# Performance work log

Measured on AMD Instinct MI355X. Metric: run time of the kernel, lower is better.

Reference implementation:

```python
import jax, jax.numpy as jnp
import numpy as np

N_CLASSES = 5
IGNORE = 255
IMAX = 32  # max instance index value (indexes in [1, IMAX])


def setup_inputs() -> dict:
    key = jax.random.key(0)
    k1, k2, k3 = jax.random.split(key, 3)
    B, D, H, W = 8, 128, 512, 512
    feature_out = jax.random.normal(k1, (B, D, H, W), dtype=jnp.float32)
    labels = jax.random.randint(k2, (B, H, W), 0, N_CLASSES).astype(jnp.int32)
    indexes = jax.random.randint(k3, (B, H, W), 1, IMAX + 1).astype(jnp.int32)
    return {"feature_out": feature_out, "labels": labels, "indexes": indexes}


def _lintra(feature_out, labels, indexes):
    # Semantics of the torch module (sort + boundary detection + python loops),
    # re-expressed as a fused segment reduction:
    #  - per-image segments are (label, instance-index) pairs among non-ignore pixels
    #  - segments with key==0 (ignore) or with a single pixel are excluded
    #  - per (image, class): instance means F [K, D], ret = mean_{i,j,d} |F_i - F_j|
    #    (includes i==j diagonal, as in the original KxK broadcast), then smooth-L1
    #  - final loss = mean over all (image, class) losses / B
    B, D, H, W = feature_out.shape
    feats = jnp.transpose(feature_out, (0, 2, 3, 1)).reshape(B * H * W, D)
    lab = labels.reshape(B, -1)
    idx = indexes.reshape(B, -1)
    valid = lab != IGNORE
    lab = jnp.where(valid, lab, 0)
    idx = jnp.where(valid, idx, 0)
    S = N_CLASSES * (IMAX + 1)
    seg = lab * (IMAX + 1) + idx                      # 0 marks ignore pixels
    gseg = (seg + jnp.arange(B, dtype=seg.dtype)[:, None] * S).reshape(-1)
    sums = jax.ops.segment_sum(feats, gseg, num_segments=B * S)
    counts = jax.ops.segment_sum(jnp.ones((B * H * W,), feats.dtype), gseg,
                                 num_segments=B * S)
    means = sums / jnp.maximum(counts, 1.0)[:, None]
    means = means.reshape(B, N_CLASSES, IMAX + 1, D)
    counts = counts.reshape(B, N_CLASSES, IMAX + 1)
    inc = counts >= 2.0                               # singleton segments skipped
    inc = inc.at[:, :, 0].set(False)                  # key==0 slot (ignore) skipped
    incf = inc.astype(means.dtype)                    # [B, C, I]
    # intra-class pairwise |F_i - F_j|, masked to included instances
    diff = jnp.abs(means[:, :, :, None, :] - means[:, :, None, :, :])  # [B,C,I,I,D]
    pair = incf[:, :, :, None] * incf[:, :, None, :]                   # [B,C,I,I]
    ssum = jnp.einsum('bcijd,bcij->bc', diff, pair)
    K = incf.sum(-1)                                   # instances per (image,class)
    ret = jnp.where(K > 0, ssum / jnp.maximum(K * K * D, 1.0), 0.0)
    loss_bc = jnp.where(ret < 1.0, 0.5 * ret * ret, ret - 0.5)
    has = (K > 0).astype(ret.dtype)
    n = has.sum()
    total = jnp.where(n > 0, (loss_bc * has).sum() / jnp.maximum(n, 1.0), 0.0)
    return (total / B).reshape(1)


def reference(feature_out, labels, indexes):
    return _lintra(feature_out, labels, indexes)
```

## Files before the change

kernel.cpp:

```cpp
#include <hip/hip_runtime.h>
#include <stdint.h>

#define NC 5
#define IMAXP1 33
#define SEGS 165
#define SEGS_PAD 192
#define MT 6
#define HW_ (512 * 512)
#define IGNORE_L 255
#define KCHUNK 2048
#define NSUP (KCHUNK / 64)

typedef __attribute__((ext_vector_type(8))) short short8v;
typedef __attribute__((ext_vector_type(16))) float f32x16;
typedef __attribute__((ext_vector_type(2))) unsigned short u16x2;
typedef __attribute__((ext_vector_type(2))) float float2v;
typedef __attribute__((ext_vector_type(2))) __bf16 bf16x2;
typedef __attribute__((ext_vector_type(2))) unsigned long long u64x2;

__global__ __launch_bounds__(256) void seg_count_kernel(
    const int* __restrict__ labels, const int* __restrict__ indexes,
    uint8_t* __restrict__ seg, unsigned* __restrict__ counts,
    int pix_per_block) {
  __shared__ unsigned hist[SEGS];
  for (int i = threadIdx.x; i < SEGS; i += blockDim.x) hist[i] = 0u;
  __syncthreads();

  const long long base = (long long)blockIdx.x * pix_per_block;
  const int b = (int)(base / HW_);
  const int nvec = pix_per_block / 4;
  const int4* lab4 = (const int4*)(labels + base);
  const int4* idx4 = (const int4*)(indexes + base);
  uchar4* seg4 = (uchar4*)(seg + base);

  for (int k = threadIdx.x; k < nvec; k += blockDim.x) {
    int4 l = lab4[k];
    int4 ix = idx4[k];
    int s0 = (l.x == IGNORE_L) ? 0 : l.x * IMAXP1 + ix.x;
    int s1 = (l.y == IGNORE_L) ? 0 : l.y * IMAXP1 + ix.y;
    int s2 = (l.z == IGNORE_L) ? 0 : l.z * IMAXP1 + ix.z;
    int s3 = (l.w == IGNORE_L) ? 0 : l.w * IMAXP1 + ix.w;
    uchar4 sv;
    sv.x = (unsigned char)s0; sv.y = (unsigned char)s1;
    sv.z = (unsigned char)s2; sv.w = (unsigned char)s3;
    seg4[k] = sv;
    atomicAdd(&hist[s0], 1u);
    atomicAdd(&hist[s1], 1u);
    atomicAdd(&hist[s2], 1u);
    atomicAdd(&hist[s3], 1u);
  }
  __syncthreads();
  for (int i = threadIdx.x; i < SEGS; i += blockDim.x)
    if (hist[i]) atomicAdd(&counts[b * SEGS + i], hist[i]);
}

struct SS {
  float4 f[8];
  u64x2 g0, g1;
};

__global__ __launch_bounds__(256, 2) void segsum_mfma_kernel(
    const float* __restrict__ feat, const uint8_t* __restrict__ seg,
    float* __restrict__ sums, int chunks_per_img) {
  __shared__ unsigned long long sseg8[KCHUNK / 8];
  const int b = blockIdx.x / chunks_per_img;
  const int chunk = blockIdx.x % chunks_per_img;
  const int pbase = chunk * KCHUNK;

  const unsigned long long* gseg8 =
      (const unsigned long long*)(seg + (size_t)b * HW_ + pbase);
  sseg8[threadIdx.x] = gseg8[threadIdx.x];
  __syncthreads();

  const int l = threadIdx.x & 63;
  const int w = threadIdx.x >> 6;
  const int lane31 = l & 31;
  const int hi = l >> 5;
  const int ch = w * 32 + lane31;

  const float4* fp4 =
      (const float4*)(feat + ((size_t)b * 128 + ch) * HW_ + pbase) + hi * 8;
  const uint8_t* sp = (const uint8_t*)sseg8 + hi * 32;

  const unsigned lane2 = (unsigned)lane31 | ((unsigned)lane31 << 16);

  f32x16 acc[MT];
  #pragma unroll
  for (int m = 0; m < MT; ++m) acc[m] = (f32x16)(0.f);

  #define LOAD_SS(dst, s)                                             \
    do {                                                              \
      _Pragma("unroll") for (int i = 0; i < 8; ++i)                   \
          (dst).f[i] = fp4[(size_t)(s)*16 + i];                       \
      const u64x2* sp2 = (const u64x2*)(sp + (s)*64);                 \
      (dst).g0 = sp2[0];                                              \
      (dst).g1 = sp2[1];                                              \
    } while (0)

  #define KSTEP(f0, f1, sb)                                           \
    do {                                                              \
      unsigned svp[4];                                                \
      _Pragma("unroll") for (int j = 0; j < 4; ++j) {                 \
        unsigned lo8 = (unsigned)(((sb) >> (16 * j)) & 0xFFull);      \
        unsigned hi8 = (unsigned)(((sb) >> (16 * j + 8)) & 0xFFull);  \
        svp[j] = (lo8 | (hi8 << 16)) ^ lane2;                         \
      }                                                               \
      float fs[8] = {(f0).x, (f0).y, (f0).z, (f0).w,                  \
                     (f1).x, (f1).y, (f1).z, (f1).w};                 \
      union { unsigned u[4]; short8v v; } bhi, blo;                   \
      _Pragma("unroll") for (int j = 0; j < 4; ++j) {                 \
        float2v f2 = {fs[2 * j], fs[2 * j + 1]};                      \
        bf16x2 h2 = __builtin_convertvector(f2, bf16x2);              \
        unsigned hb = __builtin_bit_cast(unsigned, h2);               \
        bhi.u[j] = hb;                                                \
        float fh0 = __builtin_bit_cast(float, hb << 16);              \
        float fh1 = __builtin_bit_cast(float, hb & 0xFFFF0000u);      \
        float2v l2 = {f2.x - fh0, f2.y - fh1};                        \
        bf16x2 lo2 = __builtin_convertvector(l2, bf16x2);             \
        blo.u[j] = __builtin_bit_cast(unsigned, lo2);                 \
      }                                                               \
      _Pragma("unroll") for (int m = 0; m < MT; ++m) {                \
        unsigned m2 = (unsigned)(m * 32) | ((unsigned)(m * 32) << 16);\
        union { unsigned u[4]; short8v v; } a;                        \
        _Pragma("unroll") for (int j = 0; j < 4; ++j) {               \
          u16x2 y = __builtin_bit_cast(u16x2, svp[j] ^ m2);           \
          u16x2 nz = __builtin_elementwise_min(y, (u16x2)(unsigned short)1); \
          u16x2 msk = nz - (u16x2)(unsigned short)1;                  \
          u16x2 av = msk & (u16x2)(unsigned short)0x3F80;             \
          a.u[j] = __builtin_bit_cast(unsigned, av);                  \
        }                                                             \
        acc[m] = __builtin_amdgcn_mfma_f32_32x32x16_bf16(a.v, bhi.v,  \
                                                         acc[m], 0, 0, 0); \
        acc[m] = __builtin_amdgcn_mfma_f32_32x32x16_bf16(a.v, blo.v,  \
                                                         acc[m], 0, 0, 0); \
      }                                                               \
    } while (0)

  #define COMPUTE_SS(src)                                             \
    do {                                                              \
      KSTEP((src).f[0], (src).f[1], (src).g0.x);                      \
      KSTEP((src).f[2], (src).f[3], (src).g0.y);                      \
      KSTEP((src).f[4], (src).f[5], (src).g1.x);                      \
      KSTEP((src).f[6], (src).f[7], (src).g1.y);                      \
    } while (0)

  SS bufA, bufB;
  LOAD_SS(bufA, 0);
  for (int s = 0; s < NSUP; s += 2) {
    LOAD_SS(bufB, s + 1);
    COMPUTE_SS(bufA);
    if (s + 2 < NSUP) LOAD_SS(bufA, s + 2);
    COMPUTE_SS(bufB);
  }

  #pragma unroll
  for (int m = 0; m < MT; ++m) {
    #pragma unroll
    for (int r = 0; r < 16; ++r) {
      int s = m * 32 + (r & 3) + 8 * (r >> 2) + 4 * hi;
      float v = acc[m][r];
      if (v != 0.f)
        atomicAdd(&sums[((size_t)b * SEGS_PAD + s) * 128 + ch], v);
    }
  }
}

__global__ __launch_bounds__(256) void pairloss_kernel(
    const float* __restrict__ sums, const unsigned* __restrict__ counts,
    float* __restrict__ loss_sum, unsigned* __restrict__ nvalid, int D) {
  const int b = blockIdx.x / NC;
  const int c = blockIdx.x % NC;

  __shared__ float sh_mean[32 * 128];
  __shared__ float sh_cnt[IMAXP1];
  __shared__ int list[IMAXP1];
  __shared__ int Ksh;
  __shared__ uchar2 pairs[32 * 31 / 2];
  __shared__ double wred[4];

  if (threadIdx.x == 0) {
    int K = 0;
    for (int i = 1; i < IMAXP1; ++i) {
      unsigned cnt = counts[b * SEGS + c * IMAXP1 + i];
      if (cnt >= 2u) {
        list[K] = i;
        sh_cnt[K] = (float)cnt;
        ++K;
      }
    }
    Ksh = K;
    int p = 0;
    for (int i = 0; i < K; ++i)
      for (int j = i + 1; j < K; ++j) {
        pairs[p].x = (unsigned char)i;
        pairs[p].y = (unsigned char)j;
        ++p;
      }
  }
  __syncthreads();
  const int K = Ksh;
  if (K == 0) return;

  for (int idx = threadIdx.x; idx < K * D; idx += blockDim.x) {
    int k = idx / 128, d = idx % 128;
    int s = c * IMAXP1 + list[k];
    sh_mean[k * 128 + d] =
        sums[((size_t)b * SEGS_PAD + s) * D + d] / sh_cnt[k];
  }
  __syncthreads();

  const int npairs = K * (K - 1) / 2;
  const int total = npairs * 128;
  float local = 0.f;
  for (int idx = threadIdx.x; idx < total; idx += blockDim.x) {
    int p = idx >> 7, d = idx & 127;
    int i = pairs[p].x, j = pairs[p].y;
    local += fabsf(sh_mean[i * 128 + d] - sh_mean[j * 128 + d]);
  }

  double v = (double)local;
  #pragma unroll
  for (int off = 32; off; off >>= 1) v += __shfl_down(v, off, 64);
  const int wave = threadIdx.x >> 6;
  if ((threadIdx.x & 63) == 0) wred[wave] = v;
  __syncthreads();
  if (threadIdx.x == 0) {
    double ssum = 2.0 * (wred[0] + wred[1] + wred[2] + wred[3]);
    double ret = ssum / ((double)K * (double)K * (double)D);
    double loss = (ret < 1.0) ? 0.5 * ret * ret : ret - 0.5;
    atomicAdd(loss_sum, (float)loss);
    atomicAdd(nvalid, 1u);
  }
}

__global__ void finalize_kernel(const float* __restrict__ loss_sum,
                                const unsigned* __restrict__ nvalid,
                                float* __restrict__ out, int B) {
  if (threadIdx.x == 0) {
    unsigned n = *nvalid;
    out[0] = n ? (*loss_sum / (float)n) / (float)B : 0.f;
  }
}

extern "C" void kernel_launch(void* const* d_in, const int* in_sizes, int n_in,
                              void* d_out, int out_size, void* d_ws,
                              size_t ws_size, hipStream_t stream) {
  const float* feat = (const float*)d_in[0];
  const int* labels = (const int*)d_in[1];
  const int* indexes = (const int*)d_in[2];

  const int npix_total = in_sizes[1];
  const int B = npix_total / HW_;
  const int D = in_sizes[0] / npix_total;

  uint8_t* seg = (uint8_t*)d_ws;
  size_t off = ((size_t)npix_total + 255) & ~(size_t)255;
  float* sums = (float*)((char*)d_ws + off);
  size_t sums_bytes = (size_t)B * SEGS_PAD * D * sizeof(float);
  unsigned* counts = (unsigned*)((char*)d_ws + off + sums_bytes);
  size_t counts_bytes = (size_t)B * SEGS * sizeof(unsigned);
  float* loss_sum = (float*)((char*)d_ws + off + sums_bytes + counts_bytes);
  unsigned* nvalid = (unsigned*)(loss_sum + 1);

  hipMemsetAsync(sums, 0, sums_bytes + counts_bytes + 2 * sizeof(unsigned),
                 stream);

  const int pix_per_block = 4096;
  seg_count_kernel<<<npix_total / pix_per_block, 256, 0, stream>>>(
      labels, indexes, seg, counts, pix_per_block);

  const int cpi = HW_ / KCHUNK;
  segsum_mfma_kernel<<<B * cpi, 256, 0, stream>>>(feat, seg, sums, cpi);

  pairloss_kernel<<<B * NC, 256, 0, stream>>>(sums, counts, loss_sum, nvalid,
                                              D);
  finalize_kernel<<<1, 64, 0, stream>>>(loss_sum, nvalid, (float*)d_out, B);
}
```

Before: 334.9 us.

## Replace global atomic segment accumulation with per-block partials and a reduction kernel

The MFMA segment-sum kernel now writes each block's full 192x128 accumulator tile to a per-block partials buffer instead of issuing global float atomics, and a new kernel sums the partials per image. The chunk size doubles so there are half as many blocks and partial tiles. This removes atomic contention on the shared sums array and the memset of sums, at the cost of writing and re-reading about 50 MB of partials plus an extra launch.

```diff
diff --git a/kernel.cpp b/kernel.cpp
--- a/kernel.cpp
+++ b/kernel.cpp
@@ -8,8 +8,9 @@
 #define MT 6
 #define HW_ (512 * 512)
 #define IGNORE_L 255
-#define KCHUNK 2048
+#define KCHUNK 4096
 #define NSUP (KCHUNK / 64)
+#define TILE (SEGS_PAD * 128)
 
 typedef __attribute__((ext_vector_type(8))) short short8v;
 typedef __attribute__((ext_vector_type(16))) float f32x16;
@@ -61,7 +62,7 @@
 
 __global__ __launch_bounds__(256, 2) void segsum_mfma_kernel(
     const float* __restrict__ feat, const uint8_t* __restrict__ seg,
-    float* __restrict__ sums, int chunks_per_img) {
+    float* __restrict__ partials, int chunks_per_img) {
   __shared__ unsigned long long sseg8[KCHUNK / 8];
   const int b = blockIdx.x / chunks_per_img;
   const int chunk = blockIdx.x % chunks_per_img;
@@ -69,7 +70,7 @@
 
   const unsigned long long* gseg8 =
       (const unsigned long long*)(seg + (size_t)b * HW_ + pbase);
-  sseg8[threadIdx.x] = gseg8[threadIdx.x];
+  for (int i = threadIdx.x; i < KCHUNK / 8; i += 256) sseg8[i] = gseg8[i];
   __syncthreads();
 
   const int l = threadIdx.x & 63;
@@ -153,16 +154,26 @@
     COMPUTE_SS(bufB);
   }
 
+  float* pb = partials + (size_t)blockIdx.x * TILE;
   #pragma unroll
   for (int m = 0; m < MT; ++m) {
     #pragma unroll
     for (int r = 0; r < 16; ++r) {
       int s = m * 32 + (r & 3) + 8 * (r >> 2) + 4 * hi;
-      float v = acc[m][r];
-      if (v != 0.f)
-        atomicAdd(&sums[((size_t)b * SEGS_PAD + s) * 128 + ch], v);
+      pb[s * 128 + ch] = acc[m][r];
     }
   }
+}
+
+__global__ __launch_bounds__(256) void reduce_partials_kernel(
+    const float* __restrict__ partials, float* __restrict__ sums,
+    int chunks_per_img) {
+  const int o = blockIdx.x * 256 + threadIdx.x;
+  const int b = blockIdx.y;
+  const float* p = partials + (size_t)b * chunks_per_img * TILE + o;
+  float t = 0.f;
+  for (int c = 0; c < chunks_per_img; ++c) t += p[(size_t)c * TILE];
+  sums[(size_t)b * TILE + o] = t;
 }
 
 __global__ __launch_bounds__(256) void pairloss_kernel(
@@ -205,7 +216,7 @@
     int k = idx / 128, d = idx % 128;
     int s = c * IMAXP1 + list[k];
     sh_mean[k * 128 + d] =
-        sums[((size_t)b * SEGS_PAD + s) * D + d] / sh_cnt[k];
+        sums[(size_t)b * TILE + s * 128 + d] / sh_cnt[k];
   }
   __syncthreads();
 
@@ -252,25 +263,31 @@
   const int npix_total = in_sizes[1];
   const int B = npix_total / HW_;
   const int D = in_sizes[0] / npix_total;
+  const int cpi = HW_ / KCHUNK;
+  const int nblocks = B * cpi;
 
   uint8_t* seg = (uint8_t*)d_ws;
   size_t off = ((size_t)npix_total + 255) & ~(size_t)255;
-  float* sums = (float*)((char*)d_ws + off);
-  size_t sums_bytes = (size_t)B * SEGS_PAD * D * sizeof(float);
-  unsigned* counts = (unsigned*)((char*)d_ws + off + sums_bytes);
+  float* partials = (float*)((char*)d_ws + off);
+  size_t part_bytes = (size_t)nblocks * TILE * sizeof(float);
+  float* sums = (float*)((char*)d_ws + off + part_bytes);
+  size_t sums_bytes = (size_t)B * TILE * sizeof(float);
+  unsigned* counts = (unsigned*)((char*)d_ws + off + part_bytes + sums_bytes);
   size_t counts_bytes = (size_t)B * SEGS * sizeof(unsigned);
-  float* loss_sum = (float*)((char*)d_ws + off + sums_bytes + counts_bytes);
+  float* loss_sum =
+      (float*)((char*)d_ws + off + part_bytes + sums_bytes + counts_bytes);
   unsigned* nvalid = (unsigned*)(loss_sum + 1);
 
-  hipMemsetAsync(sums, 0, sums_bytes + counts_bytes + 2 * sizeof(unsigned),
-                 stream);
+  hipMemsetAsync(counts, 0, counts_bytes + 2 * sizeof(unsigned), stream);
 
   const int pix_per_block = 4096;
   seg_count_kernel<<<npix_total / pix_per_block, 256, 0, stream>>>(
       labels, indexes, seg, counts, pix_per_block);
 
-  const int cpi = HW_ / KCHUNK;
-  segsum_mfma_kernel<<<B * cpi, 256, 0, stream>>>(feat, seg, sums, cpi);
+  segsum_mfma_kernel<<<nblocks, 256, 0, stream>>>(feat, seg, partials, cpi);
+
+  dim3 rgrid(TILE / 256, B);
+  reduce_partials_kernel<<<rgrid, 256, 0, stream>>>(partials, sums, cpi);
 
   pairloss_kernel<<<B * NC, 256, 0, stream>>>(sums, counts, loss_sum, nvalid,
                                               D);
```

New measurement: 347.1 us. 1.04x slower.

## Compact segment ids to 160 slots, drop ignore slot, cut MFMA tiles to five

Applied to the files above, without the earlier changes.

Segment ids are remapped to label*32+idx-1 so the ignore slot disappears. Ignore pixels get a 0xFF sentinel that never matches any tile, which lets the segment-sum kernel use 5 MFMA row tiles instead of 6. This removes about a sixth of the MFMA and mask-building work. The kernel also drops the shared-memory staging of segment bytes in favour of direct global loads, halves the per-stage load size, moves to triple buffering, and raises the occupancy hint to 3 blocks. The risks are register pressure under the higher occupancy bound and more uncoalesced small segment loads.

```diff
diff --git a/kernel.cpp b/kernel.cpp
--- a/kernel.cpp
+++ b/kernel.cpp
@@ -2,14 +2,14 @@
 #include <stdint.h>
 
 #define NC 5
-#define IMAXP1 33
-#define SEGS 165
-#define SEGS_PAD 192
-#define MT 6
+#define SEGS 160
+#define MT 5
 #define HW_ (512 * 512)
 #define IGNORE_L 255
+#define SENT 0xFF
 #define KCHUNK 2048
-#define NSUP (KCHUNK / 64)
+#define NSUP (KCHUNK / 32)
+#define TILE (SEGS * 128)
 
 typedef __attribute__((ext_vector_type(8))) short short8v;
 typedef __attribute__((ext_vector_type(16))) float f32x16;
@@ -22,8 +22,8 @@
     const int* __restrict__ labels, const int* __restrict__ indexes,
     uint8_t* __restrict__ seg, unsigned* __restrict__ counts,
     int pix_per_block) {
-  __shared__ unsigned hist[SEGS];
-  for (int i = threadIdx.x; i < SEGS; i += blockDim.x) hist[i] = 0u;
+  __shared__ unsigned hist[SEGS + 1];
+  for (int i = threadIdx.x; i < SEGS + 1; i += blockDim.x) hist[i] = 0u;
   __syncthreads();
 
   const long long base = (long long)blockIdx.x * pix_per_block;
@@ -36,13 +36,15 @@
   for (int k = threadIdx.x; k < nvec; k += blockDim.x) {
     int4 l = lab4[k];
     int4 ix = idx4[k];
-    int s0 = (l.x == IGNORE_L) ? 0 : l.x * IMAXP1 + ix.x;
-    int s1 = (l.y == IGNORE_L) ? 0 : l.y * IMAXP1 + ix.y;
-    int s2 = (l.z == IGNORE_L) ? 0 : l.z * IMAXP1 + ix.z;
-    int s3 = (l.w == IGNORE_L) ? 0 : l.w * IMAXP1 + ix.w;
+    int s0 = (l.x == IGNORE_L) ? SEGS : l.x * 32 + ix.x - 1;
+    int s1 = (l.y == IGNORE_L) ? SEGS : l.y * 32 + ix.y - 1;
+    int s2 = (l.z == IGNORE_L) ? SEGS : l.z * 32 + ix.z - 1;
+    int s3 = (l.w == IGNORE_L) ? SEGS : l.w * 32 + ix.w - 1;
     uchar4 sv;
-    sv.x = (unsigned char)s0; sv.y = (unsigned char)s1;
-    sv.z = (unsigned char)s2; sv.w = (unsigned char)s3;
+    sv.x = (unsigned char)(s0 == SEGS ? SENT : s0);
+    sv.y = (unsigned char)(s1 == SEGS ? SENT : s1);
+    sv.z = (unsigned char)(s2 == SEGS ? SENT : s2);
+    sv.w = (unsigned char)(s3 == SEGS ? SENT : s3);
     seg4[k] = sv;
     atomicAdd(&hist[s0], 1u);
     atomicAdd(&hist[s1], 1u);
@@ -55,22 +57,16 @@
 }
 
 struct SS {
-  float4 f[8];
-  u64x2 g0, g1;
+  float4 f[4];
+  u64x2 g;
 };
 
-__global__ __launch_bounds__(256, 2) void segsum_mfma_kernel(
+__global__ __launch_bounds__(256, 3) void segsum_mfma_kernel(
     const float* __restrict__ feat, const uint8_t* __restrict__ seg,
     float* __restrict__ sums, int chunks_per_img) {
-  __shared__ unsigned long long sseg8[KCHUNK / 8];
   const int b = blockIdx.x / chunks_per_img;
   const int chunk = blockIdx.x % chunks_per_img;
   const int pbase = chunk * KCHUNK;
-
-  const unsigned long long* gseg8 =
-      (const unsigned long long*)(seg + (size_t)b * HW_ + pbase);
-  sseg8[threadIdx.x] = gseg8[threadIdx.x];
-  __syncthreads();
 
   const int l = threadIdx.x & 63;
   const int w = threadIdx.x >> 6;
@@ -79,10 +75,15 @@
   const int ch = w * 32 + lane31;
 
   const float4* fp4 =
-      (const float4*)(feat + ((size_t)b * 128 + ch) * HW_ + pbase) + hi * 8;
-  const uint8_t* sp = (const uint8_t*)sseg8 + hi * 32;
-
-  const unsigned lane2 = (unsigned)lane31 | ((unsigned)lane31 << 16);
+      (const float4*)(feat + ((size_t)b * 128 + ch) * HW_ + pbase) + hi * 4;
+  const uint8_t* sp = seg + (size_t)b * HW_ + pbase + hi * 16;
+
+  unsigned tgt2[MT];
+  #pragma unroll
+  for (int m = 0; m < MT; ++m) {
+    unsigned t = (unsigned)(m * 32 + lane31);
+    tgt2[m] = t | (t << 16);
+  }
 
   f32x16 acc[MT];
   #pragma unroll
@@ -90,11 +91,9 @@
 
   #define LOAD_SS(dst, s)                                             \
     do {                                                              \
-      _Pragma("unroll") for (int i = 0; i < 8; ++i)                   \
-          (dst).f[i] = fp4[(size_t)(s)*16 + i];                       \
-      const u64x2* sp2 = (const u64x2*)(sp + (s)*64);                 \
-      (dst).g0 = sp2[0];                                              \
-      (dst).g1 = sp2[1];                                              \
+      _Pragma("unroll") for (int i = 0; i < 4; ++i)                   \
+          (dst).f[i] = fp4[(size_t)(s)*8 + i];                        \
+      (dst).g = *(const u64x2*)(sp + (size_t)(s)*32);                 \
     } while (0)
 
   #define KSTEP(f0, f1, sb)                                           \
@@ -103,7 +102,7 @@
       _Pragma("unroll") for (int j = 0; j < 4; ++j) {                 \
         unsigned lo8 = (unsigned)(((sb) >> (16 * j)) & 0xFFull);      \
         unsigned hi8 = (unsigned)(((sb) >> (16 * j + 8)) & 0xFFull);  \
-        svp[j] = (lo8 | (hi8 << 16)) ^ lane2;                         \
+        svp[j] = lo8 | (hi8 << 16);                                   \
       }                                                               \
       float fs[8] = {(f0).x, (f0).y, (f0).z, (f0).w,                  \
                      (f1).x, (f1).y, (f1).z, (f1).w};                 \
@@ -120,10 +119,9 @@
         blo.u[j] = __builtin_bit_cast(unsigned, lo2);                 \
       }                                                               \
       _Pragma("unroll") for (int m = 0; m < MT; ++m) {                \
-        unsigned m2 = (unsigned)(m * 32) | ((unsigned)(m * 32) << 16);\
         union { unsigned u[4]; short8v v; } a;                        \
         _Pragma("unroll") for (int j = 0; j < 4; ++j) {               \
-          u16x2 y = __builtin_bit_cast(u16x2, svp[j] ^ m2);           \
+          u16x2 y = __builtin_bit_cast(u16x2, svp[j] ^ tgt2[m]);      \
           u16x2 nz = __builtin_elementwise_min(y, (u16x2)(unsigned short)1); \
           u16x2 msk = nz - (u16x2)(unsigned short)1;                  \
           u16x2 av = msk & (u16x2)(unsigned short)0x3F80;             \
@@ -138,19 +136,20 @@
 
   #define COMPUTE_SS(src)                                             \
     do {                                                              \
-      KSTEP((src).f[0], (src).f[1], (src).g0.x);                      \
-      KSTEP((src).f[2], (src).f[3], (src).g0.y);                      \
-      KSTEP((src).f[4], (src).f[5], (src).g1.x);                      \
-      KSTEP((src).f[6], (src).f[7], (src).g1.y);                      \
+      KSTEP((src).f[0], (src).f[1], (src).g.x);                       \
+      KSTEP((src).f[2], (src).f[3], (src).g.y);                       \
     } while (0)
 
-  SS bufA, bufB;
-  LOAD_SS(bufA, 0);
-  for (int s = 0; s < NSUP; s += 2) {
-    LOAD_SS(bufB, s + 1);
-    COMPUTE_SS(bufA);
-    if (s + 2 < NSUP) LOAD_SS(bufA, s + 2);
-    COMPUTE_SS(bufB);
+  SS bA, bB, bC;
+  LOAD_SS(bA, 0);
+  LOAD_SS(bB, 1);
+  for (int s = 0; s < NSUP; s += 3) {
+    if (s + 2 < NSUP) LOAD_SS(bC, s + 2);
+    COMPUTE_SS(bA);
+    if (s + 3 < NSUP) LOAD_SS(bA, s + 3);
+    if (s + 1 < NSUP) COMPUTE_SS(bB);
+    if (s + 4 < NSUP) LOAD_SS(bB, s + 4);
+    if (s + 2 < NSUP) COMPUTE_SS(bC);
   }
 
   #pragma unroll
@@ -160,7 +159,7 @@
       int s = m * 32 + (r & 3) + 8 * (r >> 2) + 4 * hi;
       float v = acc[m][r];
       if (v != 0.f)
-        atomicAdd(&sums[((size_t)b * SEGS_PAD + s) * 128 + ch], v);
+        atomicAdd(&sums[((size_t)b * SEGS + s) * 128 + ch], v);
     }
   }
 }
@@ -172,18 +171,18 @@
   const int c = blockIdx.x % NC;
 
   __shared__ float sh_mean[32 * 128];
-  __shared__ float sh_cnt[IMAXP1];
-  __shared__ int list[IMAXP1];
+  __shared__ float sh_cnt[33];
+  __shared__ int list[33];
   __shared__ int Ksh;
   __shared__ uchar2 pairs[32 * 31 / 2];
   __shared__ double wred[4];
 
   if (threadIdx.x == 0) {
     int K = 0;
-    for (int i = 1; i < IMAXP1; ++i) {
-      unsigned cnt = counts[b * SEGS + c * IMAXP1 + i];
+    for (int ii = 0; ii < 32; ++ii) {
+      unsigned cnt = counts[b * SEGS + c * 32 + ii];
       if (cnt >= 2u) {
-        list[K] = i;
+        list[K] = ii;
         sh_cnt[K] = (float)cnt;
         ++K;
       }
@@ -203,9 +202,8 @@
 
   for (int idx = threadIdx.x; idx < K * D; idx += blockDim.x) {
     int k = idx / 128, d = idx % 128;
-    int s = c * IMAXP1 + list[k];
-    sh_mean[k * 128 + d] =
-        sums[((size_t)b * SEGS_PAD + s) * D + d] / sh_cnt[k];
+    int s = c * 32 + list[k];
+    sh_mean[k * 128 + d] = sums[((size_t)b * SEGS + s) * D + d] / sh_cnt[k];
   }
   __syncthreads();
 
@@ -252,11 +250,12 @@
   const int npix_total = in_sizes[1];
   const int B = npix_total / HW_;
   const int D = in_sizes[0] / npix_total;
+  const int cpi = HW_ / KCHUNK;
 
   uint8_t* seg = (uint8_t*)d_ws;
   size_t off = ((size_t)npix_total + 255) & ~(size_t)255;
   float* sums = (float*)((char*)d_ws + off);
-  size_t sums_bytes = (size_t)B * SEGS_PAD * D * sizeof(float);
+  size_t sums_bytes = (size_t)B * TILE * sizeof(float);
   unsigned* counts = (unsigned*)((char*)d_ws + off + sums_bytes);
   size_t counts_bytes = (size_t)B * SEGS * sizeof(unsigned);
   float* loss_sum = (float*)((char*)d_ws + off + sums_bytes + counts_bytes);
@@ -269,7 +268,6 @@
   seg_count_kernel<<<npix_total / pix_per_block, 256, 0, stream>>>(
       labels, indexes, seg, counts, pix_per_block);
 
-  const int cpi = HW_ / KCHUNK;
   segsum_mfma_kernel<<<B * cpi, 256, 0, stream>>>(feat, seg, sums, cpi);
 
   pairloss_kernel<<<B * NC, 256, 0, stream>>>(sums, counts, loss_sum, nvalid,
```

After: 448.3 us. 1.34x slower.
